# Performance work log

Hardware: AMD Instinct MI355X
Metric: run time of the kernel (lower is better)

## Reference

```python
import jax, jax.numpy as jnp
import numpy as np

ALPHA = 0.7
BETTA = 0.3
EPS = 1e-8


def _unit(v):
    n = jnp.linalg.norm(v, axis=-1, keepdims=True)
    return v / jnp.where(n > 0, n, 1.0)


def setup_inputs() -> dict:
    key = jax.random.key(0)
    k1, k2 = jax.random.split(key)
    N, D = 2097152, 3
    vec_1 = jax.random.normal(k1, (N, D), dtype=jnp.float32)
    vec_2 = jax.random.normal(k2, (N, D), dtype=jnp.float32)
    return {"vec_1": vec_1, "vec_2": vec_2}


def reference(vec_1, vec_2):
    # Row mask: keep rows where ||vec_1|| > 1e-8. Instead of boolean gather
    # (data-dependent shape), weight rows by the mask and divide by the count.
    norm1 = jnp.linalg.norm(vec_1, axis=-1, keepdims=True)  # [N,1]
    mask = (norm1 > EPS).astype(vec_1.dtype)                # [N,1]

    n1 = _unit(vec_1)                                       # [N,3]
    u2 = _unit(vec_2)
    # angle between vec_1 and vec_2 (RotationVectors.angle)
    cos_sim = jnp.clip(jnp.sum(n1 * u2, axis=-1), -1.0, 1.0)  # [N]
    a = jnp.arccos(cos_sim)
    # orthonormal companion: Gram-Schmidt of vec_2 against n1
    n2 = _unit(vec_2 - n1 * jnp.sum(n1 * vec_2, axis=-1, keepdims=True))

    sin_a = jnp.sin(a)[:, None]            # [N,1]
    cos_a_m1 = (jnp.cos(a) - 1.0)[:, None]  # [N,1]

    # bmm(M, ones) is just the row-sum of M. For M = x yT the row-sum is
    # x * sum(y), so we never materialize the [N,3,3] outer products:
    s1 = jnp.sum(n1, axis=-1, keepdims=True)  # [N,1]
    s2 = jnp.sum(n2, axis=-1, keepdims=True)
    u_ta = sin_a * (n2 * s1 - n1 * s2)        # transform_a @ ones, [N,3]
    u_tb = cos_a_m1 * (n1 * s1 + n2 * s2)     # transform_b @ ones, [N,3]
    # I @ ones == ones, so mse(I@ones, ones) == 0 elementwise.
    per_row = ALPHA * u_ta ** 2 + BETTA * u_tb ** 2  # [N,3]

    cnt = jnp.maximum(jnp.sum(mask), 1.0)
    loss = jnp.sum(per_row * mask, axis=0) / cnt     # mean over kept rows -> [3]
    return jnp.nan_to_num(loss, nan=0.0, posinf=0.1, neginf=-0.1)
```

## Files before the change

### kernel.cpp

```cpp
#include <hip/hip_runtime.h>
#include <math.h>

#define ALPHA 0.7f
#define BETTA 0.3f
#define EPS   1e-8f

#define BLOCK 256
#define RPT   4
#define TILE_ROWS (BLOCK * RPT)
#define TILE_F4   (TILE_ROWS * 3 / 4)

typedef const __attribute__((address_space(1))) void* gas_ptr;
typedef __attribute__((address_space(3))) void* las_ptr;
#define GLOAD_LDS16(gp, lp) \
    __builtin_amdgcn_global_load_lds((gas_ptr)(gp), (las_ptr)(lp), 16, 0, 0)

__device__ __forceinline__ void row_contrib(float x1, float y1, float z1,
                                            float x2, float y2, float z2,
                                            float& a0, float& a1, float& a2,
                                            float& ac) {
    float q1 = x1 * x1 + y1 * y1 + z1 * z1;
    float m = (q1 > EPS * EPS) ? 1.0f : 0.0f;
    float inv1 = (q1 > 0.0f) ? rsqrtf(q1) : 0.0f;
    float n1x = x1 * inv1, n1y = y1 * inv1, n1z = z1 * inv1;

    float q2 = x2 * x2 + y2 * y2 + z2 * z2;
    float inv2 = (q2 > 0.0f) ? rsqrtf(q2) : 0.0f;
    float u2x = x2 * inv2, u2y = y2 * inv2, u2z = z2 * inv2;

    float c = n1x * u2x + n1y * u2y + n1z * u2z;
    c = fminf(1.0f, fmaxf(-1.0f, c));
    float sin_a = sqrtf(fmaxf(0.0f, 1.0f - c * c));
    float cm1 = c - 1.0f;

    float d = n1x * x2 + n1y * y2 + n1z * z2;
    float wx = x2 - n1x * d, wy = y2 - n1y * d, wz = z2 - n1z * d;
    float wq = wx * wx + wy * wy + wz * wz;
    float invw = (wq > 0.0f) ? rsqrtf(wq) : 0.0f;
    float n2x = wx * invw, n2y = wy * invw, n2z = wz * invw;

    float s1 = n1x + n1y + n1z;
    float s2 = n2x + n2y + n2z;

    float tax = sin_a * (n2x * s1 - n1x * s2);
    float tay = sin_a * (n2y * s1 - n1y * s2);
    float taz = sin_a * (n2z * s1 - n1z * s2);

    float tbx = cm1 * (n1x * s1 + n2x * s2);
    float tby = cm1 * (n1y * s1 + n2y * s2);
    float tbz = cm1 * (n1z * s1 + n2z * s2);

    a0 += (ALPHA * tax * tax + BETTA * tbx * tbx) * m;
    a1 += (ALPHA * tay * tay + BETTA * tby * tby) * m;
    a2 += (ALPHA * taz * taz + BETTA * tbz * tbz) * m;
    ac += m;
}

__global__ __launch_bounds__(BLOCK) void trl_reduce(const float* __restrict__ v1,
                                                    const float* __restrict__ v2,
                                                    float4* __restrict__ ws,
                                                    int n_rows, int n_tiles) {
    __shared__ float4 ldsA[TILE_F4];
    __shared__ float4 ldsB[TILE_F4];

    int t = threadIdx.x;
    int lane = t & 63;
    int w = t >> 6;

    float a0 = 0.0f, a1 = 0.0f, a2 = 0.0f, ac = 0.0f;

    bool full = (blockIdx.x < (unsigned)n_tiles);
    if (full) {
        const float4* g1 = (const float4*)v1;
        const float4* g2 = (const float4*)v2;
        long base = (long)blockIdx.x * TILE_F4;
        int wslot = (w << 6);

#pragma unroll
        for (int j = 0; j < 3; ++j)
            GLOAD_LDS16(g1 + base + j * BLOCK + wslot + lane,
                        &ldsA[j * BLOCK + wslot]);
#pragma unroll
        for (int j = 0; j < 3; ++j)
            GLOAD_LDS16(g2 + base + j * BLOCK + wslot + lane,
                        &ldsB[j * BLOCK + wslot]);

        __syncthreads();

        float4 A0 = ldsA[3 * t + 0];
        float4 A1 = ldsA[3 * t + 1];
        float4 A2 = ldsA[3 * t + 2];
        float4 B0 = ldsB[3 * t + 0];
        float4 B1 = ldsB[3 * t + 1];
        float4 B2 = ldsB[3 * t + 2];

        row_contrib(A0.x, A0.y, A0.z, B0.x, B0.y, B0.z, a0, a1, a2, ac);
        row_contrib(A0.w, A1.x, A1.y, B0.w, B1.x, B1.y, a0, a1, a2, ac);
        row_contrib(A1.z, A1.w, A2.x, B1.z, B1.w, B2.x, a0, a1, a2, ac);
        row_contrib(A2.y, A2.z, A2.w, B2.y, B2.z, B2.w, a0, a1, a2, ac);
    }

    if (blockIdx.x == 0) {
        for (long r = (long)n_tiles * TILE_ROWS + t; r < n_rows; r += BLOCK) {
            const float* q1 = v1 + r * 3;
            const float* q2 = v2 + r * 3;
            row_contrib(q1[0], q1[1], q1[2], q2[0], q2[1], q2[2], a0, a1, a2, ac);
        }
    }

    for (int off = 32; off > 0; off >>= 1) {
        a0 += __shfl_down(a0, off, 64);
        a1 += __shfl_down(a1, off, 64);
        a2 += __shfl_down(a2, off, 64);
        ac += __shfl_down(ac, off, 64);
    }
    if (lane == 0) {
        float4 o;
        o.x = a0; o.y = a1; o.z = a2; o.w = ac;
        ws[(size_t)blockIdx.x * 4 + w] = o;
    }
}

__global__ __launch_bounds__(256) void trl_final(const float4* __restrict__ ws,
                                                 float* __restrict__ out,
                                                 int nparts) {
    float s0 = 0.0f, s1 = 0.0f, s2 = 0.0f, sc = 0.0f;
    for (int i = threadIdx.x; i < nparts; i += 256) {
        float4 p = ws[i];
        s0 += p.x; s1 += p.y; s2 += p.z; sc += p.w;
    }
    for (int off = 32; off > 0; off >>= 1) {
        s0 += __shfl_down(s0, off, 64);
        s1 += __shfl_down(s1, off, 64);
        s2 += __shfl_down(s2, off, 64);
        sc += __shfl_down(sc, off, 64);
    }
    __shared__ float smem[4][4];
    int lane = threadIdx.x & 63;
    int wave = threadIdx.x >> 6;
    if (lane == 0) {
        smem[wave][0] = s0;
        smem[wave][1] = s1;
        smem[wave][2] = s2;
        smem[wave][3] = sc;
    }
    __syncthreads();
    if (threadIdx.x < 3) {
        float num = smem[0][threadIdx.x] + smem[1][threadIdx.x] +
                    smem[2][threadIdx.x] + smem[3][threadIdx.x];
        float cnt = smem[0][3] + smem[1][3] + smem[2][3] + smem[3][3];
        cnt = fmaxf(cnt, 1.0f);
        float v = num / cnt;
        if (isnan(v)) v = 0.0f;
        else if (isinf(v)) v = (v > 0.0f) ? 0.1f : -0.1f;
        out[threadIdx.x] = v;
    }
}

extern "C" void kernel_launch(void* const* d_in, const int* in_sizes, int n_in,
                              void* d_out, int out_size, void* d_ws, size_t ws_size,
                              hipStream_t stream) {
    const float* v1 = (const float*)d_in[0];
    const float* v2 = (const float*)d_in[1];
    float* out = (float*)d_out;
    float4* ws = (float4*)d_ws;

    int n_rows = in_sizes[0] / 3;
    int n_tiles = n_rows / TILE_ROWS;
    int grid = (n_tiles > 0) ? n_tiles : 1;

    trl_reduce<<<grid, BLOCK, 0, stream>>>(v1, v2, ws, n_rows, n_tiles);
    trl_final<<<1, 256, 0, stream>>>(ws, out, grid * 4);
}
```

Measured before the change: 94.03 us.

## Replace LDS-direct loads with float2 register loads and two-phase padded LDS transpose

Drops the global_load_lds direct-to-LDS path. Each tile is now loaded as coalesced float2 values into registers, stored into a padded LDS layout (one pad word every 6 floats, so each thread reads its two rows at stride 7 with fewer bank conflicts), and processed in two 512-row phases. The second phase's global loads are issued before the first phase's rows are computed, to overlap memory latency with compute. The kernel also adds an occupancy hint of 8 in launch_bounds. The cost is an extra barrier pair per tile and more LDS instructions.

Measured after the change: 95.83 us. No clear change (+1.9%).

```diff
diff --git a/kernel.cpp b/kernel.cpp
--- a/kernel.cpp
+++ b/kernel.cpp
@@ -6,14 +6,11 @@
 #define EPS   1e-8f
 
 #define BLOCK 256
-#define RPT   4
-#define TILE_ROWS (BLOCK * RPT)
-#define TILE_F4   (TILE_ROWS * 3 / 4)
-
-typedef const __attribute__((address_space(1))) void* gas_ptr;
-typedef __attribute__((address_space(3))) void* las_ptr;
-#define GLOAD_LDS16(gp, lp) \
-    __builtin_amdgcn_global_load_lds((gas_ptr)(gp), (las_ptr)(lp), 16, 0, 0)
+#define TILE_ROWS  1024
+#define PHASE_ROWS 512
+#define PHASE_F2   768
+#define TILE_F2    1536
+#define LDS_DW     1792
 
 __device__ __forceinline__ void row_contrib(float x1, float y1, float z1,
                                             float x2, float y2, float z2,
@@ -56,48 +53,78 @@
     ac += m;
 }
 
-__global__ __launch_bounds__(BLOCK) void trl_reduce(const float* __restrict__ v1,
-                                                    const float* __restrict__ v2,
-                                                    float4* __restrict__ ws,
-                                                    int n_rows, int n_tiles) {
-    __shared__ float4 ldsA[TILE_F4];
-    __shared__ float4 ldsB[TILE_F4];
+__device__ __forceinline__ void lds_store_f2(float* lds, int L0, float2 v) {
+    int q = L0 / 6;
+    int p = L0 + q;
+    lds[p + 0] = v.x;
+    lds[p + 1] = v.y;
+}
+
+__global__ __launch_bounds__(BLOCK, 8) void trl_reduce(const float* __restrict__ v1,
+                                                       const float* __restrict__ v2,
+                                                       float4* __restrict__ ws,
+                                                       int n_rows, int n_tiles) {
+    __shared__ float ldsA[LDS_DW];
+    __shared__ float ldsB[LDS_DW];
 
     int t = threadIdx.x;
-    int lane = t & 63;
-    int w = t >> 6;
-
     float a0 = 0.0f, a1 = 0.0f, a2 = 0.0f, ac = 0.0f;
 
-    bool full = (blockIdx.x < (unsigned)n_tiles);
-    if (full) {
-        const float4* g1 = (const float4*)v1;
-        const float4* g2 = (const float4*)v2;
-        long base = (long)blockIdx.x * TILE_F4;
-        int wslot = (w << 6);
-
-#pragma unroll
-        for (int j = 0; j < 3; ++j)
-            GLOAD_LDS16(g1 + base + j * BLOCK + wslot + lane,
-                        &ldsA[j * BLOCK + wslot]);
-#pragma unroll
-        for (int j = 0; j < 3; ++j)
-            GLOAD_LDS16(g2 + base + j * BLOCK + wslot + lane,
-                        &ldsB[j * BLOCK + wslot]);
-
+    if (blockIdx.x < (unsigned)n_tiles) {
+        const float2* g1 = (const float2*)v1;
+        const float2* g2 = (const float2*)v2;
+        long tb = (long)blockIdx.x * TILE_F2;
+
+        float2 A0 = g1[tb + 0 * BLOCK + t];
+        float2 A1 = g1[tb + 1 * BLOCK + t];
+        float2 A2 = g1[tb + 2 * BLOCK + t];
+        float2 B0 = g2[tb + 0 * BLOCK + t];
+        float2 B1 = g2[tb + 1 * BLOCK + t];
+        float2 B2 = g2[tb + 2 * BLOCK + t];
+
+        int u = 2 * t;
+        lds_store_f2(ldsA, 0 * 512 + u, A0);
+        lds_store_f2(ldsA, 1 * 512 + u, A1);
+        lds_store_f2(ldsA, 2 * 512 + u, A2);
+        lds_store_f2(ldsB, 0 * 512 + u, B0);
+        lds_store_f2(ldsB, 1 * 512 + u, B1);
+        lds_store_f2(ldsB, 2 * 512 + u, B2);
         __syncthreads();
 
-        float4 A0 = ldsA[3 * t + 0];
-        float4 A1 = ldsA[3 * t + 1];
-        float4 A2 = ldsA[3 * t + 2];
-        float4 B0 = ldsB[3 * t + 0];
-        float4 B1 = ldsB[3 * t + 1];
-        float4 B2 = ldsB[3 * t + 2];
-
-        row_contrib(A0.x, A0.y, A0.z, B0.x, B0.y, B0.z, a0, a1, a2, ac);
-        row_contrib(A0.w, A1.x, A1.y, B0.w, B1.x, B1.y, a0, a1, a2, ac);
-        row_contrib(A1.z, A1.w, A2.x, B1.z, B1.w, B2.x, a0, a1, a2, ac);
-        row_contrib(A2.y, A2.z, A2.w, B2.y, B2.z, B2.w, a0, a1, a2, ac);
+        float fa[6], fb[6];
+        int rb = 7 * t;
+#pragma unroll
+        for (int k = 0; k < 6; ++k) fa[k] = ldsA[rb + k];
+#pragma unroll
+        for (int k = 0; k < 6; ++k) fb[k] = ldsB[rb + k];
+
+        A0 = g1[tb + PHASE_F2 + 0 * BLOCK + t];
+        A1 = g1[tb + PHASE_F2 + 1 * BLOCK + t];
+        A2 = g1[tb + PHASE_F2 + 2 * BLOCK + t];
+        B0 = g2[tb + PHASE_F2 + 0 * BLOCK + t];
+        B1 = g2[tb + PHASE_F2 + 1 * BLOCK + t];
+        B2 = g2[tb + PHASE_F2 + 2 * BLOCK + t];
+
+        row_contrib(fa[0], fa[1], fa[2], fb[0], fb[1], fb[2], a0, a1, a2, ac);
+        row_contrib(fa[3], fa[4], fa[5], fb[3], fb[4], fb[5], a0, a1, a2, ac);
+
+        __syncthreads();
+
+        lds_store_f2(ldsA, 0 * 512 + u, A0);
+        lds_store_f2(ldsA, 1 * 512 + u, A1);
+        lds_store_f2(ldsA, 2 * 512 + u, A2);
+        lds_store_f2(ldsB, 0 * 512 + u, B0);
+        lds_store_f2(ldsB, 1 * 512 + u, B1);
+        lds_store_f2(ldsB, 2 * 512 + u, B2);
+        __syncthreads();
+
+#pragma unroll
+        for (int k = 0; k < 6; ++k) fa[k] = ldsA[rb + k];
+#pragma unroll
+        for (int k = 0; k < 6; ++k) fb[k] = ldsB[rb + k];
+
+        row_contrib(fa[0], fa[1], fa[2], fb[0], fb[1], fb[2], a0, a1, a2, ac);
+        row_contrib(fa[3], fa[4], fa[5], fb[3], fb[4], fb[5], a0, a1, a2, ac);
     }
 
     if (blockIdx.x == 0) {
@@ -114,10 +141,12 @@
         a2 += __shfl_down(a2, off, 64);
         ac += __shfl_down(ac, off, 64);
     }
+    int lane = t & 63;
+    int wave = t >> 6;
     if (lane == 0) {
         float4 o;
         o.x = a0; o.y = a1; o.z = a2; o.w = ac;
-        ws[(size_t)blockIdx.x * 4 + w] = o;
+        ws[(size_t)blockIdx.x * 4 + wave] = o;
     }
 }
 
```
